# Kernel tuning notes

Measured on AMD Instinct MI355X. Metric: run time of the kernel, lower is better.

## Reference

```python
import jax, jax.numpy as jnp
import numpy as np

B, N = 512, 128
K = 3                      # top-k per row/col
CONF_THRESH = 0.05
ACCEPT_RADIUS = 0.1
CORR_THRESHOLD = 3         # min correspondences per patch
CORR_LIMIT = 2048          # verification-set size (correspondence_limit)
NUM_REFINE = 5
EPS = 1e-5


def setup_inputs() -> dict:
    key = jax.random.key(0)
    k1, k2, k3, k4, k5 = jax.random.split(key, 5)
    return {
        'score_mat': jax.random.normal(k1, (B, N, N), dtype=jnp.float32),
        'ref_knn_points': jax.random.normal(k2, (B, N, 3), dtype=jnp.float32),
        'src_knn_points': jax.random.normal(k3, (B, N, 3), dtype=jnp.float32),
        'ref_knn_masks': jax.random.bernoulli(k4, 0.95, (B, N)),
        'src_knn_masks': jax.random.bernoulli(k5, 0.95, (B, N)),
    }


def _svd_transform(H, src_c, ref_c):
    """H: (..., 3, 3) covariance; src_c/ref_c: (..., 3) centroids -> (..., 4, 4)."""
    U, _, Vh = jnp.linalg.svd(H)
    V = jnp.swapaxes(Vh, -1, -2)
    Ut = jnp.swapaxes(U, -1, -2)
    d = jnp.sign(jnp.linalg.det(V @ Ut))
    E = jnp.zeros_like(H).at[..., 0, 0].set(1.0).at[..., 1, 1].set(1.0).at[..., 2, 2].set(d)
    R = V @ E @ Ut
    t = ref_c - jnp.einsum('...ij,...j->...i', R, src_c)
    T = jnp.zeros(H.shape[:-2] + (4, 4), H.dtype)
    T = T.at[..., :3, :3].set(R).at[..., :3, 3].set(t).at[..., 3, 3].set(1.0)
    return T


def weighted_procrustes(src, ref, w):
    """src/ref: (C, 3), w: (C,) -> (4, 4). weight_thresh=0, weights >= 0 so no clamp."""
    wn = w / (jnp.sum(w, axis=-1, keepdims=True) + EPS)
    sc = jnp.einsum('n,nc->c', wn, src)
    rc = jnp.einsum('n,nc->c', wn, ref)
    H = jnp.einsum('nc,n,nd->cd', src - sc, wn, ref - rc)
    return _svd_transform(H, sc, rc)


def _topk_mask_last(scores):
    """Keep top-K values along the last axis of (B, R, S), zeros elsewhere."""
    vals, idx = jax.lax.top_k(scores, K)
    b = jnp.arange(scores.shape[0])[:, None, None]
    r = jnp.arange(scores.shape[1])[None, :, None]
    return jnp.zeros_like(scores).at[b, r, idx].set(vals)


def reference(score_mat, ref_knn_points, src_knn_points, ref_knn_masks, src_knn_masks):
    scores = jnp.exp(score_mat)  # score_mat holds log-scores (GeoTransformer forward)

    # --- correspondence matrix: dual top-k scatter + mutual + valid masks ---
    ref_corr = _topk_mask_last(scores) > CONF_THRESH
    src_corr = jnp.swapaxes(_topk_mask_last(jnp.swapaxes(scores, 1, 2)), 1, 2) > CONF_THRESH
    corr = ref_corr & src_corr  # mutual=True
    corr = corr & (ref_knn_masks[:, :, None] & src_knn_masks[:, None, :])

    masked = scores * corr.astype(scores.dtype)  # (B, N, N)
    patch_count = jnp.sum(corr, axis=(1, 2))      # correspondences per patch

    # --- per-patch weighted procrustes over all (n, m) pairs, zero-weighted pads ---
    wn = masked / (jnp.sum(masked, axis=(1, 2), keepdims=True) + EPS)
    sc = jnp.einsum('bnm,bmc->bc', wn, src_knn_points)
    rc = jnp.einsum('bnm,bnc->bc', wn, ref_knn_points)
    Hb = jnp.einsum('bnm,bmc,bnd->bcd', wn, src_knn_points - sc[:, None, :], ref_knn_points - rc[:, None, :])
    # gradients cannot flow past the boolean inlier masks below; stop_gradient avoids
    # spurious NaNs from degenerate 3x3 SVD backward on empty patches
    local_T = jax.lax.stop_gradient(_svd_transform(Hb, sc, rc))  # (B, 4, 4)

    # --- verification set: global top CORR_LIMIT correspondences ---
    flat = masked.reshape(-1)
    sel_scores, sel_idx = jax.lax.top_k(flat, CORR_LIMIT)
    b_i = sel_idx // (N * N)
    r_i = (sel_idx % (N * N)) // N
    s_i = sel_idx % N
    ref_c = ref_knn_points[b_i, r_i]  # (C, 3)
    src_c = src_knn_points[b_i, s_i]  # (C, 3)
    valid = sel_scores > 0

    # --- score every local transform by inlier count on the verification set ---
    R_all = local_T[:, :3, :3]
    t_all = local_T[:, :3, 3]
    aligned = jnp.einsum('pij,cj->pci', R_all, src_c) + t_all[:, None, :]  # (B, C, 3)
    resid = jnp.linalg.norm(ref_c[None] - aligned, axis=-1)
    inlier = (resid < ACCEPT_RADIUS) & valid[None]
    counts = jnp.where(patch_count >= CORR_THRESHOLD, jnp.sum(inlier, axis=-1), -1)
    best = jnp.argmax(counts)
    cur = sel_scores * inlier[best].astype(sel_scores.dtype)

    # --- global refinement: iterative re-weighted procrustes ---
    T = weighted_procrustes(src_c, ref_c, cur)
    for _ in range(NUM_REFINE - 1):
        aligned1 = src_c @ T[:3, :3].T + T[:3, 3]
        r1 = jnp.linalg.norm(ref_c - aligned1, axis=-1)
        cur = sel_scores * (r1 < ACCEPT_RADIUS).astype(sel_scores.dtype)
        T = weighted_procrustes(src_c, ref_c, cur)
    return T
```

## Files before the change

kernel.cpp:

```cpp
#include <hip/hip_runtime.h>
#include <math.h>

#define BB 512
#define NN 128
#define CAND_CAP (512*384)
#define LIMIT 2048
#define EQCAP 16384
#define NBIN1 4096

__device__ inline bool read_mask(const void* p, int i, int mode){
  if (mode == 0) return ((const int*)p)[i] != 0;
  if (mode == 1) return ((const unsigned char*)p)[i] != 0;
  return ((const float*)p)[i] != 0.0f;
}

__device__ inline float fast_rcp(float x){ return __builtin_amdgcn_rcpf(x); }
__device__ inline float fast_rsq(float x){ return __builtin_amdgcn_rsqf(x); }

__device__ inline void top3_update(float v, float& a1, float& a2, float& a3){
  if (v > a1){ a3=a2; a2=a1; a1=v; }
  else if (v > a2){ a3=a2; a2=v; }
  else if (v > a3){ a3=v; }
}

__device__ __forceinline__ void kabsch9(
    float h00, float h01, float h02,
    float h10, float h11, float h12,
    float h20, float h21, float h22,
    float& r00, float& r01, float& r02,
    float& r10, float& r11, float& r12,
    float& r20, float& r21, float& r22)
{
  float s00 = h00*h00 + h10*h10 + h20*h20;
  float s01 = h00*h01 + h10*h11 + h20*h21;
  float s02 = h00*h02 + h10*h12 + h20*h22;
  float s11 = h01*h01 + h11*h11 + h21*h21;
  float s12 = h01*h02 + h11*h12 + h21*h22;
  float s22 = h02*h02 + h12*h12 + h22*h22;
  float v00=1.f,v01=0.f,v02=0.f, v10=0.f,v11=1.f,v12=0.f, v20=0.f,v21=0.f,v22=1.f;
  for (int sweep = 0; sweep < 10; sweep++){
    float off  = s01*s01 + s02*s02 + s12*s12;
    float base = s00*s00 + s11*s11 + s22*s22;
    if (off <= base*1e-14f + 1e-36f) break;
    if (fabsf(s01) > 1e-30f){
      float tau = (s11 - s00) * fast_rcp(2.f*s01);
      float tt  = (tau >= 0.f ? 1.f : -1.f) * fast_rcp(fabsf(tau) + sqrtf(1.f + tau*tau));
      float c = fast_rsq(1.f + tt*tt), s = tt*c;
      float n00 = c*c*s00 - 2.f*c*s*s01 + s*s*s11;
      float n11 = s*s*s00 + 2.f*c*s*s01 + c*c*s11;
      float n02 = c*s02 - s*s12;
      float n12 = s*s02 + c*s12;
      s00=n00; s11=n11; s01=0.f; s02=n02; s12=n12;
      float a,b;
      a=v00; b=v01; v00=c*a-s*b; v01=s*a+c*b;
      a=v10; b=v11; v10=c*a-s*b; v11=s*a+c*b;
      a=v20; b=v21; v20=c*a-s*b; v21=s*a+c*b;
    }
    if (fabsf(s02) > 1e-30f){
      float tau = (s22 - s00) * fast_rcp(2.f*s02);
      float tt  = (tau >= 0.f ? 1.f : -1.f) * fast_rcp(fabsf(tau) + sqrtf(1.f + tau*tau));
      float c = fast_rsq(1.f + tt*tt), s = tt*c;
      float n00 = c*c*s00 - 2.f*c*s*s02 + s*s*s22;
      float n22 = s*s*s00 + 2.f*c*s*s02 + c*c*s22;
      float n01 = c*s01 - s*s12;
      float n12 = s*s01 + c*s12;
      s00=n00; s22=n22; s02=0.f; s01=n01; s12=n12;
      float a,b;
      a=v00; b=v02; v00=c*a-s*b; v02=s*a+c*b;
      a=v10; b=v12; v10=c*a-s*b; v12=s*a+c*b;
      a=v20; b=v22; v20=c*a-s*b; v22=s*a+c*b;
    }
    if (fabsf(s12) > 1e-30f){
      float tau = (s22 - s11) * fast_rcp(2.f*s12);
      float tt  = (tau >= 0.f ? 1.f : -1.f) * fast_rcp(fabsf(tau) + sqrtf(1.f + tau*tau));
      float c = fast_rsq(1.f + tt*tt), s = tt*c;
      float n11 = c*c*s11 - 2.f*c*s*s12 + s*s*s22;
      float n22 = s*s*s11 + 2.f*c*s*s12 + c*c*s22;
      float n01 = c*s01 - s*s02;
      float n02 = s*s01 + c*s02;
      s11=n11; s22=n22; s12=0.f; s01=n01; s02=n02;
      float a,b;
      a=v01; b=v02; v01=c*a-s*b; v02=s*a+c*b;
      a=v11; b=v12; v11=c*a-s*b; v12=s*a+c*b;
      a=v21; b=v22; v21=c*a-s*b; v22=s*a+c*b;
    }
  }
  float l0=s00, l1=s11, l2=s22;
  float a0=v00, a1=v10, a2=v20;
  float b0=v01, b1=v11, b2=v21;
  float c0=v02, c1=v12, c2=v22;
  if (l0 < l1){ float x; x=l0;l0=l1;l1=x; x=a0;a0=b0;b0=x; x=a1;a1=b1;b1=x; x=a2;a2=b2;b2=x; }
  if (l0 < l2){ float x; x=l0;l0=l2;l2=x; x=a0;a0=c0;c0=x; x=a1;a1=c1;c1=x; x=a2;a2=c2;c2=x; }
  if (l1 < l2){ float x; x=l1;l1=l2;l2=x; x=b0;b0=c0;c0=x; x=b1;b1=c1;c1=x; x=b2;b2=c2;c2=x; }
  float sig0 = sqrtf(fmaxf(l0, 0.f));
  if (!(sig0 > 1e-12f)){
    r00=1.f; r01=0.f; r02=0.f; r10=0.f; r11=1.f; r12=0.f; r20=0.f; r21=0.f; r22=1.f;
    return;
  }
  float u0x = h00*a0 + h01*a1 + h02*a2;
  float u0y = h10*a0 + h11*a1 + h12*a2;
  float u0z = h20*a0 + h21*a1 + h22*a2;
  float in0 = fast_rsq(u0x*u0x + u0y*u0y + u0z*u0z);
  u0x *= in0; u0y *= in0; u0z *= in0;
  float u1x = h00*b0 + h01*b1 + h02*b2;
  float u1y = h10*b0 + h11*b1 + h12*b2;
  float u1z = h20*b0 + h21*b1 + h22*b2;
  float dp = u1x*u0x + u1y*u0y + u1z*u0z;
  u1x -= dp*u0x; u1y -= dp*u0y; u1z -= dp*u0z;
  float d1 = u1x*u1x + u1y*u1y + u1z*u1z;
  if (sqrtf(d1) > sig0*1e-5f){
    float in1 = fast_rsq(d1);
    u1x *= in1; u1y *= in1; u1z *= in1;
  } else {
    float au0 = fabsf(u0x), au1 = fabsf(u0y), au2 = fabsf(u0z);
    float e0 = 0.f, e1 = 0.f, e2 = 0.f;
    if (au0 <= au1 && au0 <= au2) e0 = 1.f; else if (au1 <= au2) e1 = 1.f; else e2 = 1.f;
    float d2 = e0*u0x + e1*u0y + e2*u0z;
    u1x = e0 - d2*u0x; u1y = e1 - d2*u0y; u1z = e2 - d2*u0z;
    float nn = fast_rsq(u1x*u1x + u1y*u1y + u1z*u1z);
    u1x *= nn; u1y *= nn; u1z *= nn;
  }
  float u2x = u0y*u1z - u0z*u1y;
  float u2y = u0z*u1x - u0x*u1z;
  float u2z = u0x*u1y - u0y*u1x;
  float cxv = b1*c2 - b2*c1;
  float cyv = b2*c0 - b0*c2;
  float czv = b0*c1 - b1*c0;
  float detV = a0*cxv + a1*cyv + a2*czv;
  float dd = (detV >= 0.f) ? 1.f : -1.f;
  float w2x = dd*u2x, w2y = dd*u2y, w2z = dd*u2z;
  r00=a0*u0x + b0*u1x + c0*w2x;  r01=a0*u0y + b0*u1y + c0*w2y;  r02=a0*u0z + b0*u1z + c0*w2z;
  r10=a1*u0x + b1*u1x + c1*w2x;  r11=a1*u0y + b1*u1y + c1*w2y;  r12=a1*u0z + b1*u1z + c1*w2z;
  r20=a2*u0x + b2*u1x + c2*w2x;  r21=a2*u0y + b2*u1y + c2*w2y;  r22=a2*u0z + b2*u1z + c2*w2z;
}

__global__ __launch_bounds__(512, 4) void k1_kernel(
    const float* __restrict__ score, const float* __restrict__ refp,
    const float* __restrict__ srcp, const void* __restrict__ rmaskp,
    const void* __restrict__ smaskp, int* hdr, float* cand_vals, int* cand_idx,
    float* Hsr, int* pcount)
{
  __shared__ float tile[NN*NN];
  __shared__ float part[4][NN][3];
  __shared__ float c3sh[NN], r3sh[NN];
  __shared__ unsigned char smk[NN], rmk[NN];
  __shared__ float srcsh[NN*3];
  __shared__ float red[8][17];
  __shared__ int wsum[8];
  __shared__ int basesh;
  __shared__ int smode;
  const int b = blockIdx.x, t = threadIdx.x;
  const int r = t & 127, q = t >> 7;
  const int lane = t & 63, wv = t >> 6;

  if (t < 64){
    unsigned v = ((const unsigned*)rmaskp)[t];
    bool n01 = !(v == 0u || v == 1u);
    bool nf  = !(v == 0u || v == 0x3F800000u);
    unsigned long long b01 = __ballot(n01), bf = __ballot(nf);
    if (t == 0) smode = (b01 == 0ull) ? 0 : ((bf == 0ull) ? 2 : 1);
  }
  {
    const float4* s4 = (const float4*)(score + (size_t)b*NN*NN);
    float4* t4 = (float4*)tile;
    for (int j = t; j < NN*NN/4; j += 512) t4[j] = s4[j];
  }
  __syncthreads();

  if (t < NN){
    int mode = smode;
    smk[t] = read_mask(smaskp, b*NN + t, mode) ? 1 : 0;
    rmk[t] = read_mask(rmaskp, b*NN + t, mode) ? 1 : 0;
    srcsh[t*3+0] = srcp[(b*NN+t)*3+0];
    srcsh[t*3+1] = srcp[(b*NN+t)*3+1];
    srcsh[t*3+2] = srcp[(b*NN+t)*3+2];
  }
  {
    float a1=-1e30f, a2=-1e30f, a3=-1e30f;
    for (int i = 0; i < 32; i++){
      float v = tile[(q*32 + i)*NN + r];
      top3_update(v, a1, a2, a3);
    }
    part[q][r][0]=a1; part[q][r][1]=a2; part[q][r][2]=a3;
  }
  __syncthreads();
  if (t < NN){
    float m1=-1e30f, m2=-1e30f, m3=-1e30f;
#pragma unroll
    for (int qq = 0; qq < 4; qq++)
#pragma unroll
      for (int j = 0; j < 3; j++) top3_update(part[qq][t][j], m1, m2, m3);
    c3sh[t] = m3;
  }
  __syncthreads();
  {
    float a1=-1e30f, a2=-1e30f, a3=-1e30f;
    for (int i = 0; i < 32; i++){
      int c = q*32 + ((r + i) & 31);
      top3_update(tile[r*NN + c], a1, a2, a3);
    }
    part[q][r][0]=a1; part[q][r][1]=a2; part[q][r][2]=a3;
  }
  __syncthreads();
  if (t < NN){
    float m1=-1e30f, m2=-1e30f, m3=-1e30f;
#pragma unroll
    for (int qq = 0; qq < 4; qq++)
#pragma unroll
      for (int j = 0; j < 3; j++) top3_update(part[qq][t][j], m1, m2, m3);
    r3sh[t] = m3;
  }
  __syncthreads();

  float wr = 0.f, p0 = 0.f, p1 = 0.f, p2 = 0.f, cntf = 0.f;
  float kv[3]; int km[3]; int cnt = 0;
  const float r3 = r3sh[r];
  const bool rmv = rmk[r] != 0;
  const float rx = refp[(b*NN+r)*3+0], ry = refp[(b*NN+r)*3+1], rz = refp[(b*NN+r)*3+2];
  for (int i = 0; i < 32; i++){
    int c = q*32 + ((r + i) & 31);
    float v = tile[r*NN + c];
    if (rmv && smk[c] && v >= r3 && v >= c3sh[c]){
      float e = expf(v);
      if (e > 0.05f){
        cntf += 1.f; wr += e;
        p0 += e*srcsh[c*3+0]; p1 += e*srcsh[c*3+1]; p2 += e*srcsh[c*3+2];
        if (cnt < 3){ kv[cnt] = e; km[cnt] = c; cnt++; }
      }
    }
  }
  int x = cnt;
  for (int off2 = 1; off2 < 64; off2 <<= 1){ int y = __shfl_up(x, off2); if (lane >= off2) x += y; }
  if (lane == 63) wsum[wv] = x;
  __syncthreads();
  if (t == 0){
    int s2 = 0;
#pragma unroll
    for (int w = 0; w < 8; w++) s2 += wsum[w];
    basesh = atomicAdd(&hdr[0], s2);
  }
  __syncthreads();
  {
    int base = basesh + (x - cnt);
    for (int w = 0; w < wv; w++) base += wsum[w];
    for (int j = 0; j < cnt; j++){
      int pos = base + j;
      if (pos < CAND_CAP){ cand_vals[pos] = kv[j]; cand_idx[pos] = (b<<14)|(r<<7)|km[j]; }
    }
  }
  float qv[17];
  qv[0]=cntf; qv[1]=wr;
  qv[2]=wr*rx; qv[3]=wr*ry; qv[4]=wr*rz;
  qv[5]=p0; qv[6]=p1; qv[7]=p2;
  qv[8]=p0*rx;  qv[9]=p0*ry;  qv[10]=p0*rz;
  qv[11]=p1*rx; qv[12]=p1*ry; qv[13]=p1*rz;
  qv[14]=p2*rx; qv[15]=p2*ry; qv[16]=p2*rz;
#pragma unroll
  for (int k = 0; k < 17; k++){
    float v = qv[k];
    for (int off2 = 32; off2 > 0; off2 >>= 1) v += __shfl_down(v, off2);
    if (lane == 0) red[wv][k] = v;
  }
  __syncthreads();
  if (t == 0){
    float tot[17];
#pragma unroll
    for (int k = 0; k < 17; k++){
      float s2 = 0.f;
#pragma unroll
      for (int w = 0; w < 8; w++) s2 += red[w][k];
      tot[k] = s2;
    }
    float Wm = tot[1];
    float denom = Wm + 1e-5f;
    float idenom = 1.f / denom;
    float s = Wm * idenom;
    float rcv[3] = { tot[2]*idenom, tot[3]*idenom, tot[4]*idenom };
    float scv[3] = { tot[5]*idenom, tot[6]*idenom, tot[7]*idenom };
    float* o = &Hsr[b*15];
#pragma unroll
    for (int c = 0; c < 3; c++)
#pragma unroll
      for (int d = 0; d < 3; d++)
        o[c*3+d] = tot[8 + c*3 + d]*idenom - (2.f - s)*scv[c]*rcv[d];
    o[9]=scv[0]; o[10]=scv[1]; o[11]=scv[2];
    o[12]=rcv[0]; o[13]=rcv[1]; o[14]=rcv[2];
    pcount[b] = (int)(tot[0] + 0.5f);
  }
}

__global__ __launch_bounds__(256) void k3a_kernel(
    const int* hdr, const float* __restrict__ cand_vals, int* hist)
{
  __shared__ int lh[NBIN1];
  int t = threadIdx.x;
  int Nc = hdr[0]; if (Nc > CAND_CAP) Nc = CAND_CAP;
  for (int j = t; j < NBIN1; j += 256) lh[j] = 0;
  __syncthreads();
  for (int i = blockIdx.x*256 + t; i < Nc; i += gridDim.x*256)
    atomicAdd(&lh[__float_as_uint(cand_vals[i]) >> 20], 1);
  __syncthreads();
  for (int j = t; j < NBIN1; j += 256)
    if (lh[j]) atomicAdd(&hist[j], lh[j]);
}

__global__ __launch_bounds__(256) void k3c_kernel(
    int* hdr, const int* __restrict__ hist,
    const float* __restrict__ cand_vals, const int* __restrict__ cand_idx,
    float* sel_vals, int* sel_idx, float* eq_vals, int* eq_idx)
{
  __shared__ int wtot[4];
  __shared__ int sb[2];
  const int t = threadIdx.x, lane = t & 63, wv = t >> 6;
  int Nc = hdr[0]; if (Nc > CAND_CAP) Nc = CAND_CAP;
  if (Nc <= LIMIT){
    if (t == 0){ sb[0] = -1; sb[1] = 0; if (blockIdx.x == 0){ hdr[4] = -1; hdr[5] = 0; } }
    __syncthreads();
  } else {
    const int chunkIdx = 255 - t;
    int csum = 0;
    for (int j = 0; j < 16; j++) csum += hist[chunkIdx*16 + j];
    int incl = csum;
    for (int off = 1; off < 64; off <<= 1){ int y = __shfl_up(incl, off); if (lane >= off) incl += y; }
    if (lane == 63) wtot[wv] = incl;
    __syncthreads();
    int wbase = 0;
    for (int w = 0; w < wv; w++) wbase += wtot[w];
    int P = wbase + incl;
    int P_prev = P - csum;
    if (P_prev < LIMIT && P >= LIMIT){
      int cum = P_prev, bin1 = chunkIdx*16, need = 0;
      for (int b2 = chunkIdx*16 + 15; b2 >= chunkIdx*16; b2--){
        int h = hist[b2];
        if (cum + h >= LIMIT){ bin1 = b2; need = LIMIT - cum; break; }
        cum += h;
      }
      sb[0] = bin1; sb[1] = need;
      if (blockIdx.x == 0){ hdr[4] = bin1; hdr[5] = need; }
    }
    __syncthreads();
  }
  int bin1 = sb[0];
  for (int i = blockIdx.x*256 + t; i < Nc; i += gridDim.x*256){
    float v = cand_vals[i];
    if (bin1 < 0){
      int p = atomicAdd(&hdr[2], 1);
      if (p < LIMIT){ sel_vals[p] = v; sel_idx[p] = cand_idx[i]; }
      continue;
    }
    int bin = (int)(__float_as_uint(v) >> 20);
    if (bin > bin1){
      int p = atomicAdd(&hdr[2], 1);
      if (p < LIMIT){ sel_vals[p] = v; sel_idx[p] = cand_idx[i]; }
    } else if (bin == bin1){
      int q = atomicAdd(&hdr[1], 1);
      if (q < EQCAP){ eq_vals[q] = v; eq_idx[q] = cand_idx[i]; }
    }
  }
}

__global__ __launch_bounds__(1024) void k3d_kernel(
    const int* hdr, const float* __restrict__ eq_vals, const int* __restrict__ eq_idx,
    float* sel_vals, int* sel_idx,
    const float* __restrict__ refp, const float* __restrict__ srcp,
    float* sel_ref, float* sel_src)
{
  __shared__ int hist[2048];
  __shared__ int eqsh[2048];
  __shared__ int wtot[16];
  __shared__ int bpair[2];
  __shared__ int sh[2];
  const int t = threadIdx.x, lane = t & 63, wv = t >> 6;
  const int bin1 = hdr[4];
  int nAbove = hdr[2]; if (nAbove > LIMIT) nAbove = LIMIT;

  auto find_boundary = [&](int need){
    int i0 = 2047 - 2*t, i1 = 2046 - 2*t;
    int g0 = hist[i0], g1 = hist[i1];
    int local = g0 + g1;
    int incl = local;
    for (int off = 1; off < 64; off <<= 1){ int y = __shfl_up(incl, off); if (lane >= off) incl += y; }
    if (lane == 63) wtot[wv] = incl;
    __syncthreads();
    int wbase = 0;
    for (int w = 0; w < wv; w++) wbase += wtot[w];
    int P_prev = wbase + incl - local;
    int P0 = P_prev + g0;
    if (P0 >= need && P_prev < need){ bpair[0] = i0; bpair[1] = need - P_prev; }
    int P1 = P0 + g1;
    if (P1 >= need && P0 < need){ bpair[0] = i1; bpair[1] = need - P0; }
    __syncthreads();
  };

  bool done = false;
  if (bin1 < 0){
    for (int i = t; i < LIMIT; i += 1024)
      if (i >= nAbove){ sel_vals[i] = 0.f; sel_idx[i] = 0; }
    done = true;
  }
  int neq = 0, need = 0;
  if (!done){
    neq = hdr[1]; if (neq > EQCAP) neq = EQCAP;
    need = hdr[5];
    if (need >= neq){
      for (int i = t; i < neq; i += 1024){ sel_vals[nAbove+i] = eq_vals[i]; sel_idx[nAbove+i] = eq_idx[i]; }
      for (int i = t; i < LIMIT; i += 1024)
        if (i >= nAbove + neq){ sel_vals[i] = 0.f; sel_idx[i] = 0; }
      done = true;
    }
  }
  if (!done){
    for (int i = t; i < 2048; i += 1024) hist[i] = 0;
    __syncthreads();
    for (int i = t; i < neq; i += 1024)
      atomicAdd(&hist[(__float_as_uint(eq_vals[i]) >> 9) & 0x7FF], 1);
    __syncthreads();
    find_boundary(need);
    int binA = bpair[0], need2 = bpair[1];
    __syncthreads();
    for (int i = t; i < 2048; i += 1024) hist[i] = 0;
    __syncthreads();
    for (int i = t; i < neq; i += 1024){
      unsigned k = __float_as_uint(eq_vals[i]);
      if ((int)((k >> 9) & 0x7FF) == binA) atomicAdd(&hist[k & 0x1FF], 1);
    }
    __syncthreads();
    find_boundary(need2);
    unsigned Tlow = (((unsigned)binA) << 9) | (unsigned)bpair[0];
    unsigned Tkey = (((unsigned)bin1) << 20) | Tlow;
    if (t == 0){ sh[0] = 0; sh[1] = 0; }
    __syncthreads();
    for (int i = t; i < neq; i += 1024){
      unsigned k = __float_as_uint(eq_vals[i]);
      unsigned k20 = k & 0xFFFFF;
      if (k20 > Tlow){
        int p = atomicAdd(&sh[0], 1);
        sel_vals[nAbove + p] = eq_vals[i]; sel_idx[nAbove + p] = eq_idx[i];
      } else if (k20 == Tlow){
        int q = atomicAdd(&sh[1], 1);
        if (q < 2048) eqsh[q] = eq_idx[i];
      }
    }
    __syncthreads();
    if (t == 0){
      int na2 = sh[0];
      int ne2 = sh[1]; if (ne2 > 2048) ne2 = 2048;
      int take = need - na2; if (take > ne2) take = ne2; if (take < 0) take = 0;
      if (nAbove + na2 + take > LIMIT) take = LIMIT - nAbove - na2;
      for (int j = 0; j < take; j++){
        int mi = j;
        for (int l = j+1; l < ne2; l++) if (eqsh[l] < eqsh[mi]) mi = l;
        int tmp = eqsh[j]; eqsh[j] = eqsh[mi]; eqsh[mi] = tmp;
        sel_vals[nAbove + na2 + j] = __uint_as_float(Tkey);
        sel_idx[nAbove + na2 + j] = eqsh[j];
      }
      for (int j = nAbove + na2 + take; j < LIMIT; j++){ sel_vals[j] = 0.f; sel_idx[j] = 0; }
    }
  }
  __syncthreads();
  for (int p = t; p < LIMIT; p += 1024){
    int idx = sel_idx[p];
    int b = idx >> 14, rr = (idx >> 7) & 127, ss = idx & 127;
#pragma unroll
    for (int c = 0; c < 3; c++){
      sel_ref[p*3+c] = refp[(b*NN+rr)*3+c];
      sel_src[p*3+c] = srcp[(b*NN+ss)*3+c];
    }
  }
}

__global__ __launch_bounds__(256) void k45_kernel(
    const float* __restrict__ Hsr, float* __restrict__ localT,
    const float* __restrict__ sel_vals, const float* __restrict__ sel_ref,
    const float* __restrict__ sel_src, const int* __restrict__ pcount,
    int* counts, int* hdr, float* out)
{
  __shared__ float Tsh[12];
  __shared__ int ired[4];
  __shared__ int lastsh;
  __shared__ double dred[4][16];
  __shared__ long long lred[4];
  __shared__ float RT[12];
  __shared__ int sbest;
  const int b = blockIdx.x, t = threadIdx.x, lane = t & 63, wv = t >> 6;

  if (t == 0){
    const float* o = &Hsr[b*15];
    float r00,r01,r02,r10,r11,r12,r20,r21,r22;
    kabsch9(o[0],o[1],o[2], o[3],o[4],o[5], o[6],o[7],o[8],
            r00,r01,r02,r10,r11,r12,r20,r21,r22);
    Tsh[0]=r00; Tsh[1]=r01; Tsh[2]=r02;
    Tsh[3]=r10; Tsh[4]=r11; Tsh[5]=r12;
    Tsh[6]=r20; Tsh[7]=r21; Tsh[8]=r22;
    Tsh[9]  = o[12] - (r00*o[9] + r01*o[10] + r02*o[11]);
    Tsh[10] = o[13] - (r10*o[9] + r11*o[10] + r12*o[11]);
    Tsh[11] = o[14] - (r20*o[9] + r21*o[10] + r22*o[11]);
  }
  __syncthreads();
  if (t < 12) localT[b*12 + t] = Tsh[t];

  {
    float R00=Tsh[0],R01=Tsh[1],R02=Tsh[2],R10=Tsh[3],R11=Tsh[4],R12=Tsh[5];
    float R20=Tsh[6],R21=Tsh[7],R22=Tsh[8];
    float tx=Tsh[9], ty=Tsh[10], tz=Tsh[11];
    int c = 0;
    for (int p = t; p < LIMIT; p += 256){
      float v = sel_vals[p];
      if (!(v > 0.f)) continue;
      float sx=sel_src[p*3], sy=sel_src[p*3+1], sz=sel_src[p*3+2];
      float rx=sel_ref[p*3], ry=sel_ref[p*3+1], rz=sel_ref[p*3+2];
      float ax = R00*sx + R01*sy + R02*sz + tx;
      float ay = R10*sx + R11*sy + R12*sz + ty;
      float az = R20*sx + R21*sy + R22*sz + tz;
      float dx = rx-ax, dy = ry-ay, dz = rz-az;
      if (sqrtf(dx*dx + dy*dy + dz*dz) < 0.1f) c++;
    }
    for (int off2 = 32; off2 > 0; off2 >>= 1) c += __shfl_down(c, off2);
    if (lane == 0) ired[wv] = c;
    __syncthreads();
    if (t == 0){
      counts[b] = (pcount[b] >= 3) ? (ired[0]+ired[1]+ired[2]+ired[3]) : -1;
      __threadfence();
      int d = atomicAdd(&hdr[6], 1);
      lastsh = (d == BB - 1) ? 1 : 0;
    }
    __syncthreads();
    if (!lastsh) return;
    __threadfence();
  }

  {
    long long key = (long long)0x8000000000000000LL;
    for (int bb = t; bb < BB; bb += 256){
      long long kk = ((long long)(counts[bb] + 2) << 32) | (long long)(511 - bb);
      if (kk > key) key = kk;
    }
    for (int off2 = 32; off2 > 0; off2 >>= 1){ long long o = __shfl_down(key, off2); if (o > key) key = o; }
    if (lane == 0) lred[wv] = key;
    __syncthreads();
    if (t == 0){
      long long m = lred[0];
#pragma unroll
      for (int w = 1; w < 4; w++) if (lred[w] > m) m = lred[w];
      sbest = 511 - (int)(m & 0xFFFFFFFFLL);
    }
    __syncthreads();
    if (t < 12) RT[t] = localT[sbest*12 + t];
    __syncthreads();

    for (int iter = 0; iter < 5; iter++){
      float R00=RT[0],R01=RT[1],R02=RT[2];
      float R10=RT[3],R11=RT[4],R12=RT[5];
      float R20=RT[6],R21=RT[7],R22=RT[8];
      float tx=RT[9], ty=RT[10], tz=RT[11];
      double a[16];
#pragma unroll
      for (int k = 0; k < 16; k++) a[k] = 0.0;
      for (int p = t; p < LIMIT; p += 256){
        float v = sel_vals[p];
        if (!(v > 0.f)) continue;
        float sx=sel_src[p*3], sy=sel_src[p*3+1], sz=sel_src[p*3+2];
        float rx=sel_ref[p*3], ry=sel_ref[p*3+1], rz=sel_ref[p*3+2];
        float ax = R00*sx + R01*sy + R02*sz + tx;
        float ay = R10*sx + R11*sy + R12*sz + ty;
        float az = R20*sx + R21*sy + R22*sz + tz;
        float dx = rx-ax, dy = ry-ay, dz = rz-az;
        if (sqrtf(dx*dx + dy*dy + dz*dz) < 0.1f){
          double w = (double)v;
          a[0] += w;
          a[1] += w*sx; a[2] += w*sy; a[3] += w*sz;
          a[4] += w*rx; a[5] += w*ry; a[6] += w*rz;
          a[7]  += w*sx*rx; a[8]  += w*sx*ry; a[9]  += w*sx*rz;
          a[10] += w*sy*rx; a[11] += w*sy*ry; a[12] += w*sy*rz;
          a[13] += w*sz*rx; a[14] += w*sz*ry; a[15] += w*sz*rz;
        }
      }
#pragma unroll
      for (int k = 0; k < 16; k++){
        double v = a[k];
        for (int off2 = 32; off2 > 0; off2 >>= 1) v += __shfl_down(v, off2);
        if (lane == 0) dred[wv][k] = v;
      }
      __syncthreads();
      if (t == 0){
        double tot[16];
#pragma unroll
        for (int k = 0; k < 16; k++) tot[k] = dred[0][k]+dred[1][k]+dred[2][k]+dred[3][k];
        double W = tot[0], denom = W + 1e-5;
        double inv = 1.0 / denom;
        double s = W * inv;
        double scv[3] = { tot[1]*inv, tot[2]*inv, tot[3]*inv };
        double rcv[3] = { tot[4]*inv, tot[5]*inv, tot[6]*inv };
        float h00 = (float)(tot[7]*inv  - (2.0 - s)*scv[0]*rcv[0]);
        float h01 = (float)(tot[8]*inv  - (2.0 - s)*scv[0]*rcv[1]);
        float h02 = (float)(tot[9]*inv  - (2.0 - s)*scv[0]*rcv[2]);
        float h10 = (float)(tot[10]*inv - (2.0 - s)*scv[1]*rcv[0]);
        float h11 = (float)(tot[11]*inv - (2.0 - s)*scv[1]*rcv[1]);
        float h12 = (float)(tot[12]*inv - (2.0 - s)*scv[1]*rcv[2]);
        float h20 = (float)(tot[13]*inv - (2.0 - s)*scv[2]*rcv[0]);
        float h21 = (float)(tot[14]*inv - (2.0 - s)*scv[2]*rcv[1]);
        float h22 = (float)(tot[15]*inv - (2.0 - s)*scv[2]*rcv[2]);
        float r00,r01,r02,r10,r11,r12,r20,r21,r22;
        kabsch9(h00,h01,h02,h10,h11,h12,h20,h21,h22,
                r00,r01,r02,r10,r11,r12,r20,r21,r22);
        RT[0]=r00; RT[1]=r01; RT[2]=r02;
        RT[3]=r10; RT[4]=r11; RT[5]=r12;
        RT[6]=r20; RT[7]=r21; RT[8]=r22;
        RT[9]  = (float)(rcv[0] - ((double)r00*scv[0] + (double)r01*scv[1] + (double)r02*scv[2]));
        RT[10] = (float)(rcv[1] - ((double)r10*scv[0] + (double)r11*scv[1] + (double)r12*scv[2]));
        RT[11] = (float)(rcv[2] - ((double)r20*scv[0] + (double)r21*scv[1] + (double)r22*scv[2]));
      }
      __syncthreads();
    }
    if (t == 0){
      out[0]=RT[0];  out[1]=RT[1];  out[2]=RT[2];  out[3]=RT[9];
      out[4]=RT[3];  out[5]=RT[4];  out[6]=RT[5];  out[7]=RT[10];
      out[8]=RT[6];  out[9]=RT[7];  out[10]=RT[8]; out[11]=RT[11];
      out[12]=0.f; out[13]=0.f; out[14]=0.f; out[15]=1.f;
    }
  }
}

extern "C" void kernel_launch(void* const* d_in, const int* in_sizes, int n_in,
                              void* d_out, int out_size, void* d_ws, size_t ws_size,
                              hipStream_t stream){
  const float* score = (const float*)d_in[0];
  const float* refp  = (const float*)d_in[1];
  const float* srcp  = (const float*)d_in[2];
  const void*  rmask = d_in[3];
  const void*  smask = d_in[4];

  char* ws = (char*)d_ws;
  size_t off = 0;
  int* hdr = (int*)(ws + off);            off += 256;
  int* hist = (int*)(ws + off);           off += (size_t)NBIN1*4;
  float* cand_vals = (float*)(ws + off);  off += (size_t)CAND_CAP*4;
  int* cand_idx = (int*)(ws + off);       off += (size_t)CAND_CAP*4;
  float* eq_vals = (float*)(ws + off);    off += (size_t)EQCAP*4;
  int* eq_idx = (int*)(ws + off);         off += (size_t)EQCAP*4;
  float* Hsr = (float*)(ws + off);        off += (size_t)BB*15*4;
  int* pcount = (int*)(ws + off);         off += (size_t)BB*4;
  float* localT = (float*)(ws + off);     off += (size_t)BB*12*4;
  float* sel_vals = (float*)(ws + off);   off += (size_t)LIMIT*4;
  int* sel_idx = (int*)(ws + off);        off += (size_t)LIMIT*4;
  float* sel_ref = (float*)(ws + off);    off += (size_t)LIMIT*3*4;
  float* sel_src = (float*)(ws + off);    off += (size_t)LIMIT*3*4;
  int* counts = (int*)(ws + off);         off += (size_t)BB*4;

  hipMemsetAsync(ws, 0, 256 + (size_t)NBIN1*4, stream);
  hipLaunchKernelGGL(k1_kernel, dim3(BB), dim3(512), 0, stream,
                     score, refp, srcp, rmask, smask, hdr, cand_vals, cand_idx, Hsr, pcount);
  hipLaunchKernelGGL(k3a_kernel, dim3(64), dim3(256), 0, stream, hdr, cand_vals, hist);
  hipLaunchKernelGGL(k3c_kernel, dim3(64), dim3(256), 0, stream,
                     hdr, hist, cand_vals, cand_idx, sel_vals, sel_idx, eq_vals, eq_idx);
  hipLaunchKernelGGL(k3d_kernel, dim3(1), dim3(1024), 0, stream,
                     hdr, eq_vals, eq_idx, sel_vals, sel_idx, refp, srcp, sel_ref, sel_src);
  hipLaunchKernelGGL(k45_kernel, dim3(BB), dim3(256), 0, stream,
                     Hsr, localT, sel_vals, sel_ref, sel_src, pcount, counts, hdr, (float*)d_out);
}
```

Measured before the change: 257.5 us.

## Split column top-3 into separate pass, wave-shuffle row top-3, fuse histogram

The monolithic k1 kernel, which staged a 64KB score tile in shared memory, is replaced by two kernels. A light kernel computes per-column third-largest values into global memory. A second 256-thread kernel reads score rows directly, computes row top-3 with wave-level xor shuffles, and compacts candidates per wave through ballots. It also builds the value histogram inline, which removes the separate k3a histogram launch. The goal is to drop the large LDS footprint that limited occupancy and to remove a launch, at the cost of reading the score matrix twice from global memory, an extra launch for k1a, and global histogram atomics.

```diff
diff --git a/kernel.cpp b/kernel.cpp
--- a/kernel.cpp
+++ b/kernel.cpp
@@ -134,24 +134,38 @@
   r20=a2*u0x + b2*u1x + c2*w2x;  r21=a2*u0y + b2*u1y + c2*w2y;  r22=a2*u0z + b2*u1z + c2*w2z;
 }
 
-__global__ __launch_bounds__(512, 4) void k1_kernel(
+__global__ __launch_bounds__(128) void k1a_kernel(
+    const float* __restrict__ score, float* __restrict__ c3g)
+{
+  const int b = blockIdx.x, t = threadIdx.x;
+  const float* col = score + (size_t)b*NN*NN + t;
+  float a1=-1e30f, a2=-1e30f, a3=-1e30f;
+#pragma unroll 8
+  for (int n = 0; n < NN; n++){
+    float v = col[n*NN];
+    top3_update(v, a1, a2, a3);
+  }
+  c3g[b*NN + t] = a3;
+}
+
+__global__ __launch_bounds__(256) void k1b_kernel(
     const float* __restrict__ score, const float* __restrict__ refp,
     const float* __restrict__ srcp, const void* __restrict__ rmaskp,
-    const void* __restrict__ smaskp, int* hdr, float* cand_vals, int* cand_idx,
+    const void* __restrict__ smaskp, const float* __restrict__ c3g,
+    int* hdr, float* cand_vals, int* cand_idx, int* hist,
     float* Hsr, int* pcount)
 {
-  __shared__ float tile[NN*NN];
-  __shared__ float part[4][NN][3];
-  __shared__ float c3sh[NN], r3sh[NN];
+  __shared__ float srcsh[NN*3];
+  __shared__ float refsh[NN*3];
+  __shared__ float c3sh[NN];
   __shared__ unsigned char smk[NN], rmk[NN];
-  __shared__ float srcsh[NN*3];
-  __shared__ float red[8][17];
-  __shared__ int wsum[8];
-  __shared__ int basesh;
+  __shared__ float candv[4][96];
+  __shared__ int   candi[4][96];
+  __shared__ int   wcnt[4];
+  __shared__ float red[4][17];
   __shared__ int smode;
   const int b = blockIdx.x, t = threadIdx.x;
-  const int r = t & 127, q = t >> 7;
-  const int lane = t & 63, wv = t >> 6;
+  const int w = t >> 6, l = t & 63;
 
   if (t < 64){
     unsigned v = ((const unsigned*)rmaskp)[t];
@@ -160,117 +174,117 @@
     unsigned long long b01 = __ballot(n01), bf = __ballot(nf);
     if (t == 0) smode = (b01 == 0ull) ? 0 : ((bf == 0ull) ? 2 : 1);
   }
-  {
-    const float4* s4 = (const float4*)(score + (size_t)b*NN*NN);
-    float4* t4 = (float4*)tile;
-    for (int j = t; j < NN*NN/4; j += 512) t4[j] = s4[j];
-  }
+  if (t < 4) wcnt[t] = 0;
+  for (int i = t; i < NN*3; i += 256){
+    srcsh[i] = srcp[b*NN*3 + i];
+    refsh[i] = refp[b*NN*3 + i];
+  }
+  if (t < NN) c3sh[t] = c3g[b*NN + t];
   __syncthreads();
-
   if (t < NN){
     int mode = smode;
     smk[t] = read_mask(smaskp, b*NN + t, mode) ? 1 : 0;
     rmk[t] = read_mask(rmaskp, b*NN + t, mode) ? 1 : 0;
-    srcsh[t*3+0] = srcp[(b*NN+t)*3+0];
-    srcsh[t*3+1] = srcp[(b*NN+t)*3+1];
-    srcsh[t*3+2] = srcp[(b*NN+t)*3+2];
+  }
+  __syncthreads();
+
+  float q0=0.f,q1=0.f,q2=0.f,q3=0.f,q4=0.f,q5=0.f,q6=0.f,q7=0.f;
+  float q8=0.f,q9=0.f,q10=0.f,q11=0.f,q12=0.f,q13=0.f,q14=0.f,q15=0.f,q16=0.f;
+
+  const float* base = score + (size_t)b*NN*NN;
+  for (int rr = 0; rr < 32; rr++){
+    const int r = w*32 + rr;
+    const float v0 = base[r*NN + l];
+    const float v1 = base[r*NN + l + 64];
+    float a1 = fmaxf(v0, v1), a2 = fminf(v0, v1), a3 = -1e30f;
+#pragma unroll
+    for (int st = 0; st < 6; st++){
+      const int mask = 1 << st;
+      float o1 = __shfl_xor(a1, mask);
+      float o2 = __shfl_xor(a2, mask);
+      float o3 = __shfl_xor(a3, mask);
+      float m1 = fmaxf(a1, o1);
+      float m2 = fmaxf(fminf(a1, o1), fmaxf(a2, o2));
+      float m3 = fmaxf(fmaxf(fminf(a1, o2), fminf(a2, o1)), fmaxf(a3, o3));
+      a1 = m1; a2 = m2; a3 = m3;
+    }
+    const float r3 = a3;
+    const bool rmv = rmk[r] != 0;
+    const float rx = refsh[r*3+0], ry = refsh[r*3+1], rz = refsh[r*3+2];
+    float e0 = 0.f, e1 = 0.f;
+    bool k0 = false, k1 = false;
+    if (rmv && smk[l] && v0 >= r3 && v0 >= c3sh[l]){
+      e0 = expf(v0); k0 = (e0 > 0.05f);
+    }
+    if (rmv && smk[l+64] && v1 >= r3 && v1 >= c3sh[l+64]){
+      e1 = expf(v1); k1 = (e1 > 0.05f);
+    }
+    if (k0){
+      float sx = srcsh[l*3+0], sy = srcsh[l*3+1], sz = srcsh[l*3+2];
+      q0 += 1.f; q1 += e0;
+      q2 += e0*rx; q3 += e0*ry; q4 += e0*rz;
+      q5 += e0*sx; q6 += e0*sy; q7 += e0*sz;
+      q8 += e0*sx*rx;  q9 += e0*sx*ry;  q10 += e0*sx*rz;
+      q11 += e0*sy*rx; q12 += e0*sy*ry; q13 += e0*sy*rz;
+      q14 += e0*sz*rx; q15 += e0*sz*ry; q16 += e0*sz*rz;
+    }
+    if (k1){
+      int c = l + 64;
+      float sx = srcsh[c*3+0], sy = srcsh[c*3+1], sz = srcsh[c*3+2];
+      q0 += 1.f; q1 += e1;
+      q2 += e1*rx; q3 += e1*ry; q4 += e1*rz;
+      q5 += e1*sx; q6 += e1*sy; q7 += e1*sz;
+      q8 += e1*sx*rx;  q9 += e1*sx*ry;  q10 += e1*sx*rz;
+      q11 += e1*sy*rx; q12 += e1*sy*ry; q13 += e1*sy*rz;
+      q14 += e1*sz*rx; q15 += e1*sz*ry; q16 += e1*sz*rz;
+    }
+    unsigned long long B0 = __ballot(k0);
+    unsigned long long B1 = __ballot(k1);
+    int n0 = __popcll(B0), n1 = __popcll(B1);
+    if (n0 + n1 > 0){
+      int wb = 0;
+      if (l == 0){ wb = wcnt[w]; wcnt[w] = wb + n0 + n1; }
+      wb = __shfl(wb, 0);
+      unsigned long long lt = (l == 0) ? 0ull : (~0ull >> (64 - l));
+      if (k0){
+        int pos = wb + (int)__popcll(B0 & lt);
+        if (pos < 96){ candv[w][pos] = e0; candi[w][pos] = (b<<14)|(r<<7)|l; }
+      }
+      if (k1){
+        int pos = wb + n0 + (int)__popcll(B1 & lt);
+        if (pos < 96){ candv[w][pos] = e1; candi[w][pos] = (b<<14)|(r<<7)|(l+64); }
+      }
+    }
   }
   {
-    float a1=-1e30f, a2=-1e30f, a3=-1e30f;
-    for (int i = 0; i < 32; i++){
-      float v = tile[(q*32 + i)*NN + r];
-      top3_update(v, a1, a2, a3);
-    }
-    part[q][r][0]=a1; part[q][r][1]=a2; part[q][r][2]=a3;
-  }
-  __syncthreads();
-  if (t < NN){
-    float m1=-1e30f, m2=-1e30f, m3=-1e30f;
-#pragma unroll
-    for (int qq = 0; qq < 4; qq++)
-#pragma unroll
-      for (int j = 0; j < 3; j++) top3_update(part[qq][t][j], m1, m2, m3);
-    c3sh[t] = m3;
-  }
-  __syncthreads();
+    int total = wcnt[w]; if (total > 96) total = 96;
+    int gbase = 0;
+    if (l == 0 && total > 0) gbase = atomicAdd(&hdr[0], total);
+    gbase = __shfl(gbase, 0);
+    for (int i = l; i < total; i += 64){
+      float cv = candv[w][i];
+      int pos = gbase + i;
+      if (pos < CAND_CAP){
+        cand_vals[pos] = cv; cand_idx[pos] = candi[w][i];
+        atomicAdd(&hist[__float_as_uint(cv) >> 20], 1);
+      }
+    }
+  }
   {
-    float a1=-1e30f, a2=-1e30f, a3=-1e30f;
-    for (int i = 0; i < 32; i++){
-      int c = q*32 + ((r + i) & 31);
-      top3_update(tile[r*NN + c], a1, a2, a3);
-    }
-    part[q][r][0]=a1; part[q][r][1]=a2; part[q][r][2]=a3;
-  }
-  __syncthreads();
-  if (t < NN){
-    float m1=-1e30f, m2=-1e30f, m3=-1e30f;
-#pragma unroll
-    for (int qq = 0; qq < 4; qq++)
-#pragma unroll
-      for (int j = 0; j < 3; j++) top3_update(part[qq][t][j], m1, m2, m3);
-    r3sh[t] = m3;
-  }
-  __syncthreads();
-
-  float wr = 0.f, p0 = 0.f, p1 = 0.f, p2 = 0.f, cntf = 0.f;
-  float kv[3]; int km[3]; int cnt = 0;
-  const float r3 = r3sh[r];
-  const bool rmv = rmk[r] != 0;
-  const float rx = refp[(b*NN+r)*3+0], ry = refp[(b*NN+r)*3+1], rz = refp[(b*NN+r)*3+2];
-  for (int i = 0; i < 32; i++){
-    int c = q*32 + ((r + i) & 31);
-    float v = tile[r*NN + c];
-    if (rmv && smk[c] && v >= r3 && v >= c3sh[c]){
-      float e = expf(v);
-      if (e > 0.05f){
-        cntf += 1.f; wr += e;
-        p0 += e*srcsh[c*3+0]; p1 += e*srcsh[c*3+1]; p2 += e*srcsh[c*3+2];
-        if (cnt < 3){ kv[cnt] = e; km[cnt] = c; cnt++; }
-      }
-    }
-  }
-  int x = cnt;
-  for (int off2 = 1; off2 < 64; off2 <<= 1){ int y = __shfl_up(x, off2); if (lane >= off2) x += y; }
-  if (lane == 63) wsum[wv] = x;
-  __syncthreads();
-  if (t == 0){
-    int s2 = 0;
-#pragma unroll
-    for (int w = 0; w < 8; w++) s2 += wsum[w];
-    basesh = atomicAdd(&hdr[0], s2);
-  }
-  __syncthreads();
-  {
-    int base = basesh + (x - cnt);
-    for (int w = 0; w < wv; w++) base += wsum[w];
-    for (int j = 0; j < cnt; j++){
-      int pos = base + j;
-      if (pos < CAND_CAP){ cand_vals[pos] = kv[j]; cand_idx[pos] = (b<<14)|(r<<7)|km[j]; }
-    }
-  }
-  float qv[17];
-  qv[0]=cntf; qv[1]=wr;
-  qv[2]=wr*rx; qv[3]=wr*ry; qv[4]=wr*rz;
-  qv[5]=p0; qv[6]=p1; qv[7]=p2;
-  qv[8]=p0*rx;  qv[9]=p0*ry;  qv[10]=p0*rz;
-  qv[11]=p1*rx; qv[12]=p1*ry; qv[13]=p1*rz;
-  qv[14]=p2*rx; qv[15]=p2*ry; qv[16]=p2*rz;
-#pragma unroll
-  for (int k = 0; k < 17; k++){
-    float v = qv[k];
-    for (int off2 = 32; off2 > 0; off2 >>= 1) v += __shfl_down(v, off2);
-    if (lane == 0) red[wv][k] = v;
+    float qv[17] = {q0,q1,q2,q3,q4,q5,q6,q7,q8,q9,q10,q11,q12,q13,q14,q15,q16};
+#pragma unroll
+    for (int k = 0; k < 17; k++){
+      float v = qv[k];
+      for (int off2 = 32; off2 > 0; off2 >>= 1) v += __shfl_down(v, off2);
+      if (l == 0) red[w][k] = v;
+    }
   }
   __syncthreads();
   if (t == 0){
     float tot[17];
 #pragma unroll
-    for (int k = 0; k < 17; k++){
-      float s2 = 0.f;
-#pragma unroll
-      for (int w = 0; w < 8; w++) s2 += red[w][k];
-      tot[k] = s2;
-    }
+    for (int k = 0; k < 17; k++)
+      tot[k] = red[0][k] + red[1][k] + red[2][k] + red[3][k];
     float Wm = tot[1];
     float denom = Wm + 1e-5f;
     float idenom = 1.f / denom;
@@ -287,21 +301,6 @@
     o[12]=rcv[0]; o[13]=rcv[1]; o[14]=rcv[2];
     pcount[b] = (int)(tot[0] + 0.5f);
   }
-}
-
-__global__ __launch_bounds__(256) void k3a_kernel(
-    const int* hdr, const float* __restrict__ cand_vals, int* hist)
-{
-  __shared__ int lh[NBIN1];
-  int t = threadIdx.x;
-  int Nc = hdr[0]; if (Nc > CAND_CAP) Nc = CAND_CAP;
-  for (int j = t; j < NBIN1; j += 256) lh[j] = 0;
-  __syncthreads();
-  for (int i = blockIdx.x*256 + t; i < Nc; i += gridDim.x*256)
-    atomicAdd(&lh[__float_as_uint(cand_vals[i]) >> 20], 1);
-  __syncthreads();
-  for (int j = t; j < NBIN1; j += 256)
-    if (lh[j]) atomicAdd(&hist[j], lh[j]);
 }
 
 __global__ __launch_bounds__(256) void k3c_kernel(
@@ -449,7 +448,7 @@
       if (nAbove + na2 + take > LIMIT) take = LIMIT - nAbove - na2;
       for (int j = 0; j < take; j++){
         int mi = j;
-        for (int l = j+1; l < ne2; l++) if (eqsh[l] < eqsh[mi]) mi = l;
+        for (int l2 = j+1; l2 < ne2; l2++) if (eqsh[l2] < eqsh[mi]) mi = l2;
         int tmp = eqsh[j]; eqsh[j] = eqsh[mi]; eqsh[mi] = tmp;
         sel_vals[nAbove + na2 + j] = __uint_as_float(Tkey);
         sel_idx[nAbove + na2 + j] = eqsh[j];
@@ -638,6 +637,7 @@
   int* cand_idx = (int*)(ws + off);       off += (size_t)CAND_CAP*4;
   float* eq_vals = (float*)(ws + off);    off += (size_t)EQCAP*4;
   int* eq_idx = (int*)(ws + off);         off += (size_t)EQCAP*4;
+  float* c3g = (float*)(ws + off);        off += (size_t)BB*NN*4;
   float* Hsr = (float*)(ws + off);        off += (size_t)BB*15*4;
   int* pcount = (int*)(ws + off);         off += (size_t)BB*4;
   float* localT = (float*)(ws + off);     off += (size_t)BB*12*4;
@@ -648,9 +648,10 @@
   int* counts = (int*)(ws + off);         off += (size_t)BB*4;
 
   hipMemsetAsync(ws, 0, 256 + (size_t)NBIN1*4, stream);
-  hipLaunchKernelGGL(k1_kernel, dim3(BB), dim3(512), 0, stream,
-                     score, refp, srcp, rmask, smask, hdr, cand_vals, cand_idx, Hsr, pcount);
-  hipLaunchKernelGGL(k3a_kernel, dim3(64), dim3(256), 0, stream, hdr, cand_vals, hist);
+  hipLaunchKernelGGL(k1a_kernel, dim3(BB), dim3(128), 0, stream, score, c3g);
+  hipLaunchKernelGGL(k1b_kernel, dim3(BB), dim3(256), 0, stream,
+                     score, refp, srcp, rmask, smask, c3g,
+                     hdr, cand_vals, cand_idx, hist, Hsr, pcount);
   hipLaunchKernelGGL(k3c_kernel, dim3(64), dim3(256), 0, stream,
                      hdr, hist, cand_vals, cand_idx, sel_vals, sel_idx, eq_vals, eq_idx);
   hipLaunchKernelGGL(k3d_kernel, dim3(1), dim3(1024), 0, stream,
```

After: 653.6 us. 2.54x slower.
